# Performance work log

Measured on AMD Instinct MI355X. Metric: run time of the kernel, lower is better.

The kernel has to match this reference:

```python
import jax, jax.numpy as jnp
import numpy as np

N_SRC, N_DST, E = 10000, 10000, 640000
S, T, O, H = 128, 128, 128, 4
D = O // H


def setup_inputs() -> dict:
    key = jax.random.key(0)
    ks = jax.random.split(key, 12)
    f = lambda k, shape, fan: jax.random.normal(k, shape, dtype=jnp.float32) / np.float32(np.sqrt(fan))
    return {
        "x_src": jax.random.normal(ks[0], (N_SRC, S), dtype=jnp.float32),
        "x_dst": jax.random.normal(ks[1], (N_DST, T), dtype=jnp.float32),
        "W_pred1": f(ks[2], (S, T), T),
        "b_pred1": jnp.zeros((S,), jnp.float32),
        "W_pred2": f(ks[3], (S, S), S),
        "b_pred2": jnp.zeros((S,), jnp.float32),
        "W_res": f(ks[4], (H * D, S), S),
        "W_src": f(ks[5], (H * D, S), S),
        "W_dst": f(ks[6], (H * D, T), T),
        "att_src": jax.random.normal(ks[7], (1, H, D), dtype=jnp.float32) * 0.01,
        "att_dst": jax.random.normal(ks[8], (1, H, D), dtype=jnp.float32) * 0.01,
        "W_self": f(ks[9], (H * D, T), T),
        "b_self": jnp.zeros((H * D,), jnp.float32),
        "edge_src": jax.random.randint(ks[10], (E,), 0, N_SRC),
        "edge_dst": jax.random.randint(ks[11], (E,), 0, N_DST),
        "num_dst": N_DST,
    }


def reference(x_src, x_dst, W_pred1, b_pred1, W_pred2, b_pred2, W_res, W_src, W_dst,
              att_src, att_dst, W_self, b_self, edge_src, edge_dst, num_dst):
    h, d = att_src.shape[1], att_src.shape[2]
    # residual prediction path: pred_mlp(x_dst) = Lin2(ReLU(Lin1(x_dst)))
    pred = jax.nn.relu(x_dst @ W_pred1.T + b_pred1) @ W_pred2.T + b_pred2  # [Ndst,S]
    residual = x_src[edge_src] - pred[edge_dst]                            # [E,S]
    # per-node attention logits (equivalent to gather-then-dot, cheaper)
    a_s = ((x_src @ W_src.T).reshape(-1, h, d) * att_src).sum(-1)          # [Nsrc,H]
    a_d = ((x_dst @ W_dst.T).reshape(-1, h, d) * att_dst).sum(-1)          # [Ndst,H]
    alpha = jax.nn.leaky_relu(a_s[edge_src] + a_d[edge_dst], 0.2)          # [E,H]
    # edge softmax over incoming edges of each destination node
    amax = jax.ops.segment_max(alpha, edge_dst, num_segments=num_dst)      # [Ndst,H]
    ex = jnp.exp(alpha - amax[edge_dst])
    denom = jax.ops.segment_sum(ex, edge_dst, num_segments=num_dst)
    alpha = ex / (denom[edge_dst] + 1e-16)                                 # [E,H]
    # attention-weighted aggregation of transformed residuals
    msg = (residual @ W_res.T).reshape(-1, h, d) * alpha[:, :, None]       # [E,H,D]
    agg = jax.ops.segment_sum(msg.reshape(-1, h * d), edge_dst, num_segments=num_dst)
    return agg + x_dst @ W_self.T + b_self                                 # [Ndst,H*D]
```

## Files before the change

kernel.cpp:

```cpp
#include <hip/hip_runtime.h>

#define LEAKY 0.2f
#define CAP 160
#define CAPB 8192
#define CHUNK 2048
#define GSTRIDE 32

#define FMA4(A, S, V) do { (A).x += (S)*(V).x; (A).y += (S)*(V).y; (A).z += (S)*(V).z; (A).w += (S)*(V).w; } while (0)

struct GemmJob { const float* X; const float* W; const float* B; float* Y; int M; int relu; int bf16out; };

__device__ __forceinline__ unsigned short f2bf(float f) {
  unsigned int u = __float_as_uint(f);
  u += 0x7FFFu + ((u >> 16) & 1u);
  return (unsigned short)(u >> 16);
}
__device__ __forceinline__ float bf2f(unsigned short h) {
  return __uint_as_float(((unsigned int)h) << 16);
}

__device__ __forceinline__ void gemm128_block(
    const float* __restrict__ X, const float* __restrict__ W,
    const float* __restrict__ B, float* __restrict__ Y,
    int M, int relu, int bf16out, int row0,
    float* __restrict__ XsT , float* __restrict__ WTs ) {
  if (row0 >= M) return;
  const int tid = threadIdx.x;
  const int tx = tid & 15;
  const int ty = tid >> 4;
  float4 acc[8][2];
#pragma unroll
  for (int i = 0; i < 8; i++) {
    acc[i][0] = make_float4(0.f, 0.f, 0.f, 0.f);
    acc[i][1] = make_float4(0.f, 0.f, 0.f, 0.f);
  }
  const int rS = tid >> 1;
  const int kb = (tid & 1) * 8;

  for (int k0 = 0; k0 < 128; k0 += 16) {
    int rr = row0 + rS; if (rr >= M) rr = M - 1;
    const float* xp = X + (size_t)rr * 128 + k0 + kb;
    float4 a0 = *(const float4*)xp;
    float4 a1 = *(const float4*)(xp + 4);
    XsT[(kb + 0) * 128 + rS] = a0.x; XsT[(kb + 1) * 128 + rS] = a0.y;
    XsT[(kb + 2) * 128 + rS] = a0.z; XsT[(kb + 3) * 128 + rS] = a0.w;
    XsT[(kb + 4) * 128 + rS] = a1.x; XsT[(kb + 5) * 128 + rS] = a1.y;
    XsT[(kb + 6) * 128 + rS] = a1.z; XsT[(kb + 7) * 128 + rS] = a1.w;

    const float* wp = W + (size_t)rS * 128 + k0 + kb;
    float4 b0 = *(const float4*)wp;
    float4 b1 = *(const float4*)(wp + 4);
    WTs[(kb + 0) * 128 + rS] = b0.x; WTs[(kb + 1) * 128 + rS] = b0.y;
    WTs[(kb + 2) * 128 + rS] = b0.z; WTs[(kb + 3) * 128 + rS] = b0.w;
    WTs[(kb + 4) * 128 + rS] = b1.x; WTs[(kb + 5) * 128 + rS] = b1.y;
    WTs[(kb + 6) * 128 + rS] = b1.z; WTs[(kb + 7) * 128 + rS] = b1.w;
    __syncthreads();

#pragma unroll
    for (int k = 0; k < 16; k++) {
      float4 xa = *(const float4*)&XsT[k * 128 + ty * 4];
      float4 xb = *(const float4*)&XsT[k * 128 + 64 + ty * 4];
      float4 w0 = *(const float4*)&WTs[k * 128 + tx * 4];
      float4 w1 = *(const float4*)&WTs[k * 128 + 64 + tx * 4];
      FMA4(acc[0][0], xa.x, w0); FMA4(acc[0][1], xa.x, w1);
      FMA4(acc[1][0], xa.y, w0); FMA4(acc[1][1], xa.y, w1);
      FMA4(acc[2][0], xa.z, w0); FMA4(acc[2][1], xa.z, w1);
      FMA4(acc[3][0], xa.w, w0); FMA4(acc[3][1], xa.w, w1);
      FMA4(acc[4][0], xb.x, w0); FMA4(acc[4][1], xb.x, w1);
      FMA4(acc[5][0], xb.y, w0); FMA4(acc[5][1], xb.y, w1);
      FMA4(acc[6][0], xb.z, w0); FMA4(acc[6][1], xb.z, w1);
      FMA4(acc[7][0], xb.w, w0); FMA4(acc[7][1], xb.w, w1);
    }
    __syncthreads();
  }

  float4 bv0 = make_float4(0.f, 0.f, 0.f, 0.f);
  float4 bv1 = make_float4(0.f, 0.f, 0.f, 0.f);
  if (B) { bv0 = *(const float4*)(B + tx * 4); bv1 = *(const float4*)(B + 64 + tx * 4); }
#pragma unroll
  for (int i = 0; i < 8; i++) {
    int r = row0 + (i < 4 ? ty * 4 + i : 64 + ty * 4 + (i - 4));
    if (r < M) {
      float4 o0, o1;
      o0.x = acc[i][0].x + bv0.x; o0.y = acc[i][0].y + bv0.y;
      o0.z = acc[i][0].z + bv0.z; o0.w = acc[i][0].w + bv0.w;
      o1.x = acc[i][1].x + bv1.x; o1.y = acc[i][1].y + bv1.y;
      o1.z = acc[i][1].z + bv1.z; o1.w = acc[i][1].w + bv1.w;
      if (relu) {
        o0.x = fmaxf(o0.x, 0.f); o0.y = fmaxf(o0.y, 0.f);
        o0.z = fmaxf(o0.z, 0.f); o0.w = fmaxf(o0.w, 0.f);
        o1.x = fmaxf(o1.x, 0.f); o1.y = fmaxf(o1.y, 0.f);
        o1.z = fmaxf(o1.z, 0.f); o1.w = fmaxf(o1.w, 0.f);
      }
      if (bf16out) {
        unsigned short* yb = (unsigned short*)Y;
        ushort4 p0, p1;
        p0.x = f2bf(o0.x); p0.y = f2bf(o0.y); p0.z = f2bf(o0.z); p0.w = f2bf(o0.w);
        p1.x = f2bf(o1.x); p1.y = f2bf(o1.y); p1.z = f2bf(o1.z); p1.w = f2bf(o1.w);
        *(ushort4*)(yb + (size_t)r * 128 + tx * 4) = p0;
        *(ushort4*)(yb + (size_t)r * 128 + 64 + tx * 4) = p1;
      } else {
        *(float4*)(Y + (size_t)r * 128 + tx * 4) = o0;
        *(float4*)(Y + (size_t)r * 128 + 64 + tx * 4) = o1;
      }
    }
  }
}

__device__ __forceinline__ void attn32_block(const float* __restrict__ X,
                                             const float* __restrict__ v,
                                             float* __restrict__ a, int M, int blk,
                                             float* __restrict__ vsf ) {
  int tid = threadIdx.x;
  for (int i = tid; i < 512; i += 256) vsf[i + ((i >> 5) << 2)] = v[i];
  __syncthreads();
  int g = tid >> 3, l = tid & 7;
  int n = blk * 32 + g;
  if (n >= M) return;
  const float* xp = X + (size_t)n * 128 + l * 16;
  float4 x0 = *(const float4*)xp;
  float4 x1 = *(const float4*)(xp + 4);
  float4 x2 = *(const float4*)(xp + 8);
  float4 x3 = *(const float4*)(xp + 12);
  const float4* vv = (const float4*)vsf;
  int s = l * 18;
  float4 p = make_float4(0.f, 0.f, 0.f, 0.f);
  FMA4(p, x0.x, vv[s + 0]); FMA4(p, x0.y, vv[s + 1]); FMA4(p, x0.z, vv[s + 2]); FMA4(p, x0.w, vv[s + 3]);
  FMA4(p, x1.x, vv[s + 4]); FMA4(p, x1.y, vv[s + 5]); FMA4(p, x1.z, vv[s + 6]); FMA4(p, x1.w, vv[s + 7]);
  FMA4(p, x2.x, vv[s + 9]); FMA4(p, x2.y, vv[s +10]); FMA4(p, x2.z, vv[s +11]); FMA4(p, x2.w, vv[s +12]);
  FMA4(p, x3.x, vv[s +13]); FMA4(p, x3.y, vv[s +14]); FMA4(p, x3.z, vv[s +15]); FMA4(p, x3.w, vv[s +16]);
#pragma unroll
  for (int off = 1; off < 8; off <<= 1) {
    p.x += __shfl_xor(p.x, off, 64);
    p.y += __shfl_xor(p.y, off, 64);
    p.z += __shfl_xor(p.z, off, 64);
    p.w += __shfl_xor(p.w, off, 64);
  }
  if (l == 0) *(float4*)(a + (size_t)n * 4) = p;
}

__global__ __launch_bounds__(256) void phase1(
    const float* __restrict__ Wsrc, const float* __restrict__ attsrc,
    const float* __restrict__ Wdst, const float* __restrict__ attdst,
    const float* __restrict__ W_res, const float* __restrict__ W2,
    const float* __restrict__ b2,
    GemmJob jA,
    float* __restrict__ v_src, float* __restrict__ v_dst,
    float* __restrict__ Wc, float* __restrict__ bc,
    const int* __restrict__ edge_src, const int* __restrict__ edge_dst,
    int* __restrict__ gcnt, int* __restrict__ bin,
    int E, int Nd, int NB, int GA, int Q1, int T1) {
  __shared__ float smem[4096];
  int bx = blockIdx.x, tid = threadIdx.x;
  int u = (bx & 7) * Q1 + (bx >> 3);
  if (u >= T1) return;
  if (u == 0) {
    int which = tid >> 7, k = tid & 127;
    const float* W = which ? Wdst : Wsrc;
    const float* att = which ? attdst : attsrc;
    float* v = which ? v_dst : v_src;
    float s[4] = {0.f, 0.f, 0.f, 0.f};
#pragma unroll
    for (int h = 0; h < 4; h++)
      for (int d = 0; d < 32; d++)
        s[h] += W[(size_t)(h * 32 + d) * 128 + k] * att[h * 32 + d];
#pragma unroll
    for (int h = 0; h < 4; h++) v[k * 4 + h] = s[h];
  } else if (u == 1) {
    if (tid < 128) {
      float s = 0.f;
      for (int i = 0; i < 128; i++) s += W_res[(size_t)tid * 128 + i] * b2[i];
      bc[tid] = s;
    }
  } else if (u < 66) {
    int id = (u - 2) * 256 + tid;
    int o = id >> 7, j = id & 127;
    float s = 0.f;
    for (int i = 0; i < 128; i++) s += W_res[(size_t)o * 128 + i] * W2[(size_t)i * 128 + j];
    Wc[(size_t)o * 128 + j] = s;
  } else if (u < 66 + GA) {
    gemm128_block(jA.X, jA.W, jA.B, jA.Y, jA.M, jA.relu, jA.bf16out,
                  (u - 66) * 128, smem, smem + 2048);
  } else {
    int* pk    = (int*)smem;
    int* hist  = (int*)smem + CHUNK;
    int* gbase = hist + 160;
    int* lcur  = gbase + 160;
    int e0 = (u - 66 - GA) * CHUNK;
    int n = E - e0; if (n > CHUNK) n = CHUNK;
    if (n <= 0) return;
    for (int i = tid; i < NB; i += 256) hist[i] = 0;
    __syncthreads();
    for (int i = tid; i < n; i += 256) {
      int s = edge_src[e0 + i], d = edge_dst[e0 + i];
      pk[i] = (s << 14) | d;
      atomicAdd(&hist[d >> 6], 1);
    }
    __syncthreads();
    for (int b = tid; b < NB; b += 256) {
      gbase[b] = hist[b] ? atomicAdd(&gcnt[b * GSTRIDE], hist[b]) : 0;
      lcur[b] = 0;
    }
    __syncthreads();
    for (int i = tid; i < n; i += 256) {
      int p = pk[i];
      int b = (p & 16383) >> 6;
      int off = gbase[b] + atomicAdd(&lcur[b], 1);
      if (off < CAPB) bin[(size_t)b * CAPB + off] = p;
    }
  }
}

__global__ __launch_bounds__(256) void phase2(
    GemmJob j0, GemmJob j1, GemmJob j2,
    const float* __restrict__ x_src, const float* __restrict__ x_dst,
    const float* __restrict__ v_src, const float* __restrict__ v_dst,
    float* __restrict__ a_s, float* __restrict__ a_d,
    const int* __restrict__ gcnt, const int* __restrict__ bin,
    int* __restrict__ sorted_src, int* __restrict__ rstart, int* __restrict__ rend,
    int Ns, int Nd, int NB, int G, int As, int Ad, int Q2, int T2) {
  __shared__ float smem[4096];
  int bx = blockIdx.x, tid = threadIdx.x;
  int u = (bx % 6) * Q2 + bx / 6;
  if (u >= T2) return;
  if (u < 3 * G) {
    GemmJob J = (u < G) ? j0 : (u < 2 * G) ? j1 : j2;
    gemm128_block(J.X, J.W, J.B, J.Y, J.M, J.relu, J.bf16out, (u % G) * 128, smem, smem + 2048);
  } else if (u < 3 * G + As) {
    attn32_block(x_src, v_src, a_s, Ns, u - 3 * G, smem);
  } else if (u < 3 * G + As + Ad) {
    attn32_block(x_dst, v_dst, a_d, Nd, u - 3 * G - As, smem);
  } else {
    int b = u - (3 * G + As + Ad);
    int* hist2 = (int*)smem;
    int* lcur2 = (int*)smem + 64;
    int cnt = gcnt[b * GSTRIDE]; if (cnt > CAPB) cnt = CAPB;
    size_t base = (size_t)b * CAPB;
    if (tid < 64) hist2[tid] = 0;
    __syncthreads();
    for (int i = tid; i < cnt; i += 256) atomicAdd(&hist2[bin[base + i] & 63], 1);
    __syncthreads();
    if (tid < 64) {
      int v = hist2[tid];
      int incl = v;
#pragma unroll
      for (int off = 1; off < 64; off <<= 1) {
        int t = __shfl_up(incl, off, 64);
        if (tid >= off) incl += t;
      }
      int st = incl - v;
      lcur2[tid] = st;
      int dst = (b << 6) + tid;
      if (dst < Nd) {
        rstart[dst] = (int)base + st;
        rend[dst]   = (int)base + st + v;
      }
    }
    __syncthreads();
    for (int i = tid; i < cnt; i += 256) {
      int p = bin[base + i];
      int j = p & 63;
      int lp = atomicAdd(&lcur2[j], 1);
      sorted_src[base + lp] = p >> 14;
    }
  }
}

__global__ __launch_bounds__(256) void phase3(
    const int* __restrict__ rstart, const int* __restrict__ rend,
    const int* __restrict__ sorted_src,
    const float* __restrict__ a_s, const float* __restrict__ a_d,
    const unsigned short* __restrict__ u_src, const float* __restrict__ u_pred,
    const float* __restrict__ self_o, float* __restrict__ out, int Nd) {
  __shared__ float smem[1920];
  int bx = blockIdx.x, tid = threadIdx.x;
  int half = tid >> 7;
  int t = tid & 127;
  int dst = bx * 2 + half;
  if (dst >= Nd) return;

  float* wbuf  = smem + half * 640;
  int* srcbuf  = (int*)(smem + 1280) + half * 160;
  float4* red4 = (float4*)(smem + 1600);
  float4* redv = (float4*)(smem + 1616) + half * 32;
  float* inv_s = smem + 1872 + half * 4;
  float* sA_s  = smem + 1880 + half * 4;

  int start = rstart[dst];
  int deg = rend[dst] - start;
  float4 ad4 = *(const float4*)(a_d + (size_t)dst * 4);
  float s0 = 0.f, s1 = 0.f, s2 = 0.f, s3 = 0.f;
  for (int i = t; i < deg; i += 128) {
    int src = sorted_src[start + i];
    float4 as4 = *(const float4*)(a_s + (size_t)src * 4);
    float l0 = as4.x + ad4.x; l0 = l0 > 0.f ? l0 : LEAKY * l0;
    float l1 = as4.y + ad4.y; l1 = l1 > 0.f ? l1 : LEAKY * l1;
    float l2 = as4.z + ad4.z; l2 = l2 > 0.f ? l2 : LEAKY * l2;
    float l3 = as4.w + ad4.w; l3 = l3 > 0.f ? l3 : LEAKY * l3;
    float w0 = __expf(l0), w1 = __expf(l1), w2 = __expf(l2), w3 = __expf(l3);
    if (i < CAP) {
      wbuf[i * 4 + 0] = w0; wbuf[i * 4 + 1] = w1;
      wbuf[i * 4 + 2] = w2; wbuf[i * 4 + 3] = w3;
      srcbuf[i] = src;
    }
    s0 += w0; s1 += w1; s2 += w2; s3 += w3;
  }
  int wave = tid >> 6;
#pragma unroll
  for (int off = 32; off > 0; off >>= 1) {
    s0 += __shfl_xor(s0, off, 64);
    s1 += __shfl_xor(s1, off, 64);
    s2 += __shfl_xor(s2, off, 64);
    s3 += __shfl_xor(s3, off, 64);
  }
  if ((tid & 63) == 0) red4[wave] = make_float4(s0, s1, s2, s3);
  __syncthreads();
  if (t == 0) {
    float4 A = red4[half * 2], B = red4[half * 2 + 1];
    float dx = A.x + B.x, dy = A.y + B.y, dz = A.z + B.z, dw = A.w + B.w;
    inv_s[0] = 1.f / (dx + 1e-16f); sA_s[0] = dx * inv_s[0];
    inv_s[1] = 1.f / (dy + 1e-16f); sA_s[1] = dy * inv_s[1];
    inv_s[2] = 1.f / (dz + 1e-16f); sA_s[2] = dz * inv_s[2];
    inv_s[3] = 1.f / (dw + 1e-16f); sA_s[3] = dw * inv_s[3];
  }
  __syncthreads();

  int c4 = t & 31, rgrp = t >> 5, h = c4 >> 3;
  int coff = c4 * 4;
  float4 acc0 = make_float4(0.f,0.f,0.f,0.f), acc1 = acc0, acc2 = acc0, acc3 = acc0;
  int cap = deg < CAP ? deg : CAP;
  int i = rgrp;
  for (; i + 12 < cap; i += 16) {
    int sA = srcbuf[i], sB = srcbuf[i + 4], sC = srcbuf[i + 8], sD = srcbuf[i + 12];
    float wA = wbuf[i * 4 + h], wB = wbuf[(i + 4) * 4 + h];
    float wC = wbuf[(i + 8) * 4 + h], wD = wbuf[(i + 12) * 4 + h];
    ushort4 hA = *(const ushort4*)(u_src + (size_t)sA * 128 + coff);
    ushort4 hB = *(const ushort4*)(u_src + (size_t)sB * 128 + coff);
    ushort4 hC = *(const ushort4*)(u_src + (size_t)sC * 128 + coff);
    ushort4 hD = *(const ushort4*)(u_src + (size_t)sD * 128 + coff);
    float4 uA = make_float4(bf2f(hA.x), bf2f(hA.y), bf2f(hA.z), bf2f(hA.w));
    float4 uB = make_float4(bf2f(hB.x), bf2f(hB.y), bf2f(hB.z), bf2f(hB.w));
    float4 uC = make_float4(bf2f(hC.x), bf2f(hC.y), bf2f(hC.z), bf2f(hC.w));
    float4 uD = make_float4(bf2f(hD.x), bf2f(hD.y), bf2f(hD.z), bf2f(hD.w));
    FMA4(acc0, wA, uA); FMA4(acc1, wB, uB); FMA4(acc2, wC, uC); FMA4(acc3, wD, uD);
  }
  for (; i < cap; i += 4) {
    int s_ = srcbuf[i];
    float w = wbuf[i * 4 + h];
    ushort4 hh = *(const ushort4*)(u_src + (size_t)s_ * 128 + coff);
    float4 uu = make_float4(bf2f(hh.x), bf2f(hh.y), bf2f(hh.z), bf2f(hh.w));
    FMA4(acc0, w, uu);
  }
  if (deg > CAP) {
    float adh = (h == 0) ? ad4.x : (h == 1) ? ad4.y : (h == 2) ? ad4.z : ad4.w;
    for (int k = CAP + rgrp; k < deg; k += 4) {
      int src = sorted_src[start + k];
      float l = a_s[(size_t)src * 4 + h] + adh;
      l = l > 0.f ? l : LEAKY * l;
      float w = __expf(l);
      ushort4 hh = *(const ushort4*)(u_src + (size_t)src * 128 + coff);
      float4 uu = make_float4(bf2f(hh.x), bf2f(hh.y), bf2f(hh.z), bf2f(hh.w));
      FMA4(acc0, w, uu);
    }
  }
  float4 acc;
  acc.x = acc0.x + acc1.x + acc2.x + acc3.x;
  acc.y = acc0.y + acc1.y + acc2.y + acc3.y;
  acc.z = acc0.z + acc1.z + acc2.z + acc3.z;
  acc.w = acc0.w + acc1.w + acc2.w + acc3.w;
  acc.x += __shfl_xor(acc.x, 32, 64);
  acc.y += __shfl_xor(acc.y, 32, 64);
  acc.z += __shfl_xor(acc.z, 32, 64);
  acc.w += __shfl_xor(acc.w, 32, 64);
  if (t >= 64 && t < 96) redv[c4] = acc;
  __syncthreads();
  if (t < 32) {
    float4 r = redv[c4];
    acc.x += r.x; acc.y += r.y; acc.z += r.z; acc.w += r.w;
    float4 up = *(const float4*)(u_pred + (size_t)dst * 128 + coff);
    float4 so = *(const float4*)(self_o + (size_t)dst * 128 + coff);
    float iv = inv_s[h], sa = sA_s[h];
    float4 o;
    o.x = acc.x * iv - sa * up.x + so.x;
    o.y = acc.y * iv - sa * up.y + so.y;
    o.z = acc.z * iv - sa * up.z + so.z;
    o.w = acc.w * iv - sa * up.w + so.w;
    *(float4*)(out + (size_t)dst * 128 + coff) = o;
  }
}

extern "C" void kernel_launch(void* const* d_in, const int* in_sizes, int n_in,
                              void* d_out, int out_size, void* d_ws, size_t ws_size,
                              hipStream_t stream) {
  const float* x_src   = (const float*)d_in[0];
  const float* x_dst   = (const float*)d_in[1];
  const float* W_pred1 = (const float*)d_in[2];
  const float* b_pred1 = (const float*)d_in[3];
  const float* W_pred2 = (const float*)d_in[4];
  const float* b_pred2 = (const float*)d_in[5];
  const float* W_res   = (const float*)d_in[6];
  const float* W_src   = (const float*)d_in[7];
  const float* W_dst   = (const float*)d_in[8];
  const float* att_src = (const float*)d_in[9];
  const float* att_dst = (const float*)d_in[10];
  const float* W_self  = (const float*)d_in[11];
  const float* b_self  = (const float*)d_in[12];
  const int* edge_src  = (const int*)d_in[13];
  const int* edge_dst  = (const int*)d_in[14];
  int Ns = in_sizes[0] / 128;
  int Nd = in_sizes[1] / 128;
  int E  = in_sizes[13];
  float* out = (float*)d_out;
  int NB = (Nd + 63) >> 6;

  char* ws = (char*)d_ws;
  auto alloc = [&](size_t bytes) -> char* {
    char* p = ws;
    ws += (bytes + 255) & ~(size_t)255;
    return p;
  };
  float* relu1  = (float*)alloc((size_t)Nd * 128 * 4);
  unsigned short* u_src = (unsigned short*)alloc((size_t)Ns * 128 * 2);
  float* u_pred = (float*)alloc((size_t)Nd * 128 * 4);
  float* self_o = (float*)alloc((size_t)Nd * 128 * 4);
  float* a_s    = (float*)alloc((size_t)Ns * 4 * 4);
  float* a_d    = (float*)alloc((size_t)Nd * 4 * 4);
  float* v_src  = (float*)alloc(128 * 4 * 4);
  float* v_dst  = (float*)alloc(128 * 4 * 4);
  float* Wc     = (float*)alloc(128 * 128 * 4);
  float* bc     = (float*)alloc(128 * 4);
  int* gcnt     = (int*)alloc((size_t)NB * GSTRIDE * 4);
  int* rstart   = (int*)alloc((size_t)Nd * 4);
  int* rend     = (int*)alloc((size_t)Nd * 4);
  int* bin      = (int*)alloc((size_t)NB * CAPB * 4);
  int* sorted_src = (int*)alloc((size_t)NB * CAPB * 4);

  hipMemsetAsync(gcnt, 0, (size_t)NB * GSTRIDE * sizeof(int), stream);

  int GA  = (Nd + 127) / 128;
  int NCH = (E + CHUNK - 1) / CHUNK;
  int T1 = 66 + GA + NCH;
  int Q1 = (T1 + 7) / 8;
  GemmJob jA{ x_dst, W_pred1, b_pred1, relu1, Nd, 1, 0 };
  hipLaunchKernelGGL(phase1, dim3(Q1 * 8), dim3(256), 0, stream,
                     W_src, att_src, W_dst, att_dst, W_res, W_pred2, b_pred2, jA,
                     v_src, v_dst, Wc, bc, edge_src, edge_dst, gcnt, bin,
                     E, Nd, NB, GA, Q1, T1);

  int maxM = Ns > Nd ? Ns : Nd;
  int G  = (maxM + 127) / 128;
  int As = (Ns + 31) / 32;
  int Ad = (Nd + 31) / 32;
  int T2 = 3 * G + As + Ad + NB;
  int Q2 = (T2 + 5) / 6;
  GemmJob jB{ x_src, W_res,  nullptr, (float*)u_src, Ns, 0, 1 };
  GemmJob jC{ x_dst, W_self, b_self,  self_o, Nd, 0, 0 };
  GemmJob jU{ relu1, Wc,     bc,      u_pred, Nd, 0, 0 };
  hipLaunchKernelGGL(phase2, dim3(Q2 * 6), dim3(256), 0, stream,
                     jB, jC, jU, x_src, x_dst, v_src, v_dst, a_s, a_d,
                     gcnt, bin, sorted_src, rstart, rend,
                     Ns, Nd, NB, G, As, Ad, Q2, T2);

  hipLaunchKernelGGL(phase3, dim3((Nd + 1) / 2), dim3(256), 0, stream,
                     rstart, rend, sorted_src, a_s, a_d, u_src, u_pred, self_o, out, Nd);
}
```

Measured before the change: 166.2 us.

## Switch dense GEMMs to bf16 MFMA and fuse attention logits into GEMM

Replaces the LDS-tiled fp32 FMA GEMM with a register-only bf16 MFMA (16x16x32) GEMM that loads X and W straight from global memory and converts them to bf16 in registers. The per-node attention-logit dot products (a_s, a_d) are computed inside the x_src and x_dst GEMM blocks from the same X loads, which removes the separate attn32 blocks and their second read of X. Shared-memory use in both kernels shrinks, which may allow more resident blocks. In exchange, GEMM inputs lose precision through bf16 rounding, and the output stores are now scalar and strided instead of float4.

```diff
diff --git a/kernel.cpp b/kernel.cpp
--- a/kernel.cpp
+++ b/kernel.cpp
@@ -1,4 +1,5 @@
 #include <hip/hip_runtime.h>
+#include <hip/hip_bf16.h>
 
 #define LEAKY 0.2f
 #define CAP 160
@@ -8,7 +9,15 @@
 
 #define FMA4(A, S, V) do { (A).x += (S)*(V).x; (A).y += (S)*(V).y; (A).z += (S)*(V).z; (A).w += (S)*(V).w; } while (0)
 
-struct GemmJob { const float* X; const float* W; const float* B; float* Y; int M; int relu; int bf16out; };
+typedef __attribute__((ext_vector_type(8))) short bf16x8;
+typedef __attribute__((ext_vector_type(4))) float f32x4;
+
+struct GemmJob {
+  const float* X; const float* W; const float* B; float* Y;
+  int M; int relu; int bf16out;
+  const float* vvec;
+  float* aout;
+};
 
 __device__ __forceinline__ unsigned short f2bf(float f) {
   unsigned int u = __float_as_uint(f);
@@ -19,124 +28,127 @@
   return __uint_as_float(((unsigned int)h) << 16);
 }
 
-__device__ __forceinline__ void gemm128_block(
+__device__ __forceinline__ bf16x8 pack8(const float4& a, const float4& b) {
+  bf16x8 r;
+  r[0] = (short)__builtin_bit_cast(unsigned short, __float2bfloat16(a.x));
+  r[1] = (short)__builtin_bit_cast(unsigned short, __float2bfloat16(a.y));
+  r[2] = (short)__builtin_bit_cast(unsigned short, __float2bfloat16(a.z));
+  r[3] = (short)__builtin_bit_cast(unsigned short, __float2bfloat16(a.w));
+  r[4] = (short)__builtin_bit_cast(unsigned short, __float2bfloat16(b.x));
+  r[5] = (short)__builtin_bit_cast(unsigned short, __float2bfloat16(b.y));
+  r[6] = (short)__builtin_bit_cast(unsigned short, __float2bfloat16(b.z));
+  r[7] = (short)__builtin_bit_cast(unsigned short, __float2bfloat16(b.w));
+  return r;
+}
+
+__device__ __forceinline__ void gemm128_mfma(
     const float* __restrict__ X, const float* __restrict__ W,
     const float* __restrict__ B, float* __restrict__ Y,
     int M, int relu, int bf16out, int row0,
-    float* __restrict__ XsT , float* __restrict__ WTs ) {
+    const float* __restrict__ vvec, float* __restrict__ aout) {
   if (row0 >= M) return;
   const int tid = threadIdx.x;
-  const int tx = tid & 15;
-  const int ty = tid >> 4;
-  float4 acc[8][2];
-#pragma unroll
-  for (int i = 0; i < 8; i++) {
-    acc[i][0] = make_float4(0.f, 0.f, 0.f, 0.f);
-    acc[i][1] = make_float4(0.f, 0.f, 0.f, 0.f);
-  }
-  const int rS = tid >> 1;
-  const int kb = (tid & 1) * 8;
-
-  for (int k0 = 0; k0 < 128; k0 += 16) {
-    int rr = row0 + rS; if (rr >= M) rr = M - 1;
-    const float* xp = X + (size_t)rr * 128 + k0 + kb;
-    float4 a0 = *(const float4*)xp;
-    float4 a1 = *(const float4*)(xp + 4);
-    XsT[(kb + 0) * 128 + rS] = a0.x; XsT[(kb + 1) * 128 + rS] = a0.y;
-    XsT[(kb + 2) * 128 + rS] = a0.z; XsT[(kb + 3) * 128 + rS] = a0.w;
-    XsT[(kb + 4) * 128 + rS] = a1.x; XsT[(kb + 5) * 128 + rS] = a1.y;
-    XsT[(kb + 6) * 128 + rS] = a1.z; XsT[(kb + 7) * 128 + rS] = a1.w;
-
-    const float* wp = W + (size_t)rS * 128 + k0 + kb;
-    float4 b0 = *(const float4*)wp;
-    float4 b1 = *(const float4*)(wp + 4);
-    WTs[(kb + 0) * 128 + rS] = b0.x; WTs[(kb + 1) * 128 + rS] = b0.y;
-    WTs[(kb + 2) * 128 + rS] = b0.z; WTs[(kb + 3) * 128 + rS] = b0.w;
-    WTs[(kb + 4) * 128 + rS] = b1.x; WTs[(kb + 5) * 128 + rS] = b1.y;
-    WTs[(kb + 6) * 128 + rS] = b1.z; WTs[(kb + 7) * 128 + rS] = b1.w;
-    __syncthreads();
-
-#pragma unroll
-    for (int k = 0; k < 16; k++) {
-      float4 xa = *(const float4*)&XsT[k * 128 + ty * 4];
-      float4 xb = *(const float4*)&XsT[k * 128 + 64 + ty * 4];
-      float4 w0 = *(const float4*)&WTs[k * 128 + tx * 4];
-      float4 w1 = *(const float4*)&WTs[k * 128 + 64 + tx * 4];
-      FMA4(acc[0][0], xa.x, w0); FMA4(acc[0][1], xa.x, w1);
-      FMA4(acc[1][0], xa.y, w0); FMA4(acc[1][1], xa.y, w1);
-      FMA4(acc[2][0], xa.z, w0); FMA4(acc[2][1], xa.z, w1);
-      FMA4(acc[3][0], xa.w, w0); FMA4(acc[3][1], xa.w, w1);
-      FMA4(acc[4][0], xb.x, w0); FMA4(acc[4][1], xb.x, w1);
-      FMA4(acc[5][0], xb.y, w0); FMA4(acc[5][1], xb.y, w1);
-      FMA4(acc[6][0], xb.z, w0); FMA4(acc[6][1], xb.z, w1);
-      FMA4(acc[7][0], xb.w, w0); FMA4(acc[7][1], xb.w, w1);
-    }
-    __syncthreads();
-  }
-
-  float4 bv0 = make_float4(0.f, 0.f, 0.f, 0.f);
-  float4 bv1 = make_float4(0.f, 0.f, 0.f, 0.f);
-  if (B) { bv0 = *(const float4*)(B + tx * 4); bv1 = *(const float4*)(B + 64 + tx * 4); }
-#pragma unroll
-  for (int i = 0; i < 8; i++) {
-    int r = row0 + (i < 4 ? ty * 4 + i : 64 + ty * 4 + (i - 4));
-    if (r < M) {
-      float4 o0, o1;
-      o0.x = acc[i][0].x + bv0.x; o0.y = acc[i][0].y + bv0.y;
-      o0.z = acc[i][0].z + bv0.z; o0.w = acc[i][0].w + bv0.w;
-      o1.x = acc[i][1].x + bv1.x; o1.y = acc[i][1].y + bv1.y;
-      o1.z = acc[i][1].z + bv1.z; o1.w = acc[i][1].w + bv1.w;
-      if (relu) {
-        o0.x = fmaxf(o0.x, 0.f); o0.y = fmaxf(o0.y, 0.f);
-        o0.z = fmaxf(o0.z, 0.f); o0.w = fmaxf(o0.w, 0.f);
-        o1.x = fmaxf(o1.x, 0.f); o1.y = fmaxf(o1.y, 0.f);
-        o1.z = fmaxf(o1.z, 0.f); o1.w = fmaxf(o1.w, 0.f);
+  const int wv = tid >> 6;
+  const int ln = tid & 63;
+  const int lr = ln & 15;
+  const int kg = ln >> 4;
+
+  const f32x4 zero = {0.f, 0.f, 0.f, 0.f};
+  f32x4 acc[2][8];
+#pragma unroll
+  for (int mt = 0; mt < 2; mt++)
+#pragma unroll
+    for (int nt = 0; nt < 8; nt++) acc[mt][nt] = zero;
+
+  float4 av0 = make_float4(0.f, 0.f, 0.f, 0.f), av1 = av0;
+
+  const int r0 = row0 + wv * 32 + lr;
+  const int r1 = r0 + 16;
+  const int rc0 = r0 < M ? r0 : M - 1;
+  const int rc1 = r1 < M ? r1 : M - 1;
+  const float* xp0 = X + (size_t)rc0 * 128 + kg * 8;
+  const float* xp1 = X + (size_t)rc1 * 128 + kg * 8;
+  const float* wp  = W + (size_t)lr * 128 + kg * 8;
+
+#pragma unroll
+  for (int k0 = 0; k0 < 128; k0 += 32) {
+    float4 xa0 = *(const float4*)(xp0 + k0);
+    float4 xb0 = *(const float4*)(xp0 + k0 + 4);
+    float4 xa1 = *(const float4*)(xp1 + k0);
+    float4 xb1 = *(const float4*)(xp1 + k0 + 4);
+    bf16x8 a0 = pack8(xa0, xb0);
+    bf16x8 a1 = pack8(xa1, xb1);
+#pragma unroll
+    for (int nt = 0; nt < 8; nt++) {
+      const float* wq = wp + (size_t)nt * 16 * 128 + k0;
+      bf16x8 bw = pack8(*(const float4*)wq, *(const float4*)(wq + 4));
+      acc[0][nt] = __builtin_amdgcn_mfma_f32_16x16x32_bf16(a0, bw, acc[0][nt], 0, 0, 0);
+      acc[1][nt] = __builtin_amdgcn_mfma_f32_16x16x32_bf16(a1, bw, acc[1][nt], 0, 0, 0);
+    }
+    if (vvec) {
+      const float4* vv = (const float4*)vvec + (k0 + kg * 8);
+#pragma unroll
+      for (int j = 0; j < 4; j++) {
+        float4 v4 = vv[j];
+        float s0 = (j == 0) ? xa0.x : (j == 1) ? xa0.y : (j == 2) ? xa0.z : xa0.w;
+        float s1 = (j == 0) ? xa1.x : (j == 1) ? xa1.y : (j == 2) ? xa1.z : xa1.w;
+        FMA4(av0, s0, v4); FMA4(av1, s1, v4);
       }
+#pragma unroll
+      for (int j = 0; j < 4; j++) {
+        float4 v4 = vv[4 + j];
+        float s0 = (j == 0) ? xb0.x : (j == 1) ? xb0.y : (j == 2) ? xb0.z : xb0.w;
+        float s1 = (j == 0) ? xb1.x : (j == 1) ? xb1.y : (j == 2) ? xb1.z : xb1.w;
+        FMA4(av0, s0, v4); FMA4(av1, s1, v4);
+      }
+    }
+  }
+
+  if (vvec) {
+    av0.x += __shfl_xor(av0.x, 16, 64); av0.y += __shfl_xor(av0.y, 16, 64);
+    av0.z += __shfl_xor(av0.z, 16, 64); av0.w += __shfl_xor(av0.w, 16, 64);
+    av0.x += __shfl_xor(av0.x, 32, 64); av0.y += __shfl_xor(av0.y, 32, 64);
+    av0.z += __shfl_xor(av0.z, 32, 64); av0.w += __shfl_xor(av0.w, 32, 64);
+    av1.x += __shfl_xor(av1.x, 16, 64); av1.y += __shfl_xor(av1.y, 16, 64);
+    av1.z += __shfl_xor(av1.z, 16, 64); av1.w += __shfl_xor(av1.w, 16, 64);
+    av1.x += __shfl_xor(av1.x, 32, 64); av1.y += __shfl_xor(av1.y, 32, 64);
+    av1.z += __shfl_xor(av1.z, 32, 64); av1.w += __shfl_xor(av1.w, 32, 64);
+    if (kg == 0) {
+      if (r0 < M) *(float4*)(aout + (size_t)r0 * 4) = av0;
+      if (r1 < M) *(float4*)(aout + (size_t)r1 * 4) = av1;
+    }
+  }
+
+  float bv[8];
+#pragma unroll
+  for (int nt = 0; nt < 8; nt++) bv[nt] = B ? B[nt * 16 + lr] : 0.f;
+
+  const int rbase = row0 + wv * 32 + kg * 4;
+#pragma unroll
+  for (int mt = 0; mt < 2; mt++) {
+#pragma unroll
+    for (int i = 0; i < 4; i++) {
+      int r = rbase + mt * 16 + i;
+      if (r >= M) continue;
       if (bf16out) {
-        unsigned short* yb = (unsigned short*)Y;
-        ushort4 p0, p1;
-        p0.x = f2bf(o0.x); p0.y = f2bf(o0.y); p0.z = f2bf(o0.z); p0.w = f2bf(o0.w);
-        p1.x = f2bf(o1.x); p1.y = f2bf(o1.y); p1.z = f2bf(o1.z); p1.w = f2bf(o1.w);
-        *(ushort4*)(yb + (size_t)r * 128 + tx * 4) = p0;
-        *(ushort4*)(yb + (size_t)r * 128 + 64 + tx * 4) = p1;
+        unsigned short* yb = (unsigned short*)Y + (size_t)r * 128 + lr;
+#pragma unroll
+        for (int nt = 0; nt < 8; nt++) {
+          float o = acc[mt][nt][i] + bv[nt];
+          if (relu) o = fmaxf(o, 0.f);
+          yb[nt * 16] = f2bf(o);
+        }
       } else {
-        *(float4*)(Y + (size_t)r * 128 + tx * 4) = o0;
-        *(float4*)(Y + (size_t)r * 128 + 64 + tx * 4) = o1;
+        float* yp = Y + (size_t)r * 128 + lr;
+#pragma unroll
+        for (int nt = 0; nt < 8; nt++) {
+          float o = acc[mt][nt][i] + bv[nt];
+          if (relu) o = fmaxf(o, 0.f);
+          yp[nt * 16] = o;
+        }
       }
     }
   }
-}
-
-__device__ __forceinline__ void attn32_block(const float* __restrict__ X,
-                                             const float* __restrict__ v,
-                                             float* __restrict__ a, int M, int blk,
-                                             float* __restrict__ vsf ) {
-  int tid = threadIdx.x;
-  for (int i = tid; i < 512; i += 256) vsf[i + ((i >> 5) << 2)] = v[i];
-  __syncthreads();
-  int g = tid >> 3, l = tid & 7;
-  int n = blk * 32 + g;
-  if (n >= M) return;
-  const float* xp = X + (size_t)n * 128 + l * 16;
-  float4 x0 = *(const float4*)xp;
-  float4 x1 = *(const float4*)(xp + 4);
-  float4 x2 = *(const float4*)(xp + 8);
-  float4 x3 = *(const float4*)(xp + 12);
-  const float4* vv = (const float4*)vsf;
-  int s = l * 18;
-  float4 p = make_float4(0.f, 0.f, 0.f, 0.f);
-  FMA4(p, x0.x, vv[s + 0]); FMA4(p, x0.y, vv[s + 1]); FMA4(p, x0.z, vv[s + 2]); FMA4(p, x0.w, vv[s + 3]);
-  FMA4(p, x1.x, vv[s + 4]); FMA4(p, x1.y, vv[s + 5]); FMA4(p, x1.z, vv[s + 6]); FMA4(p, x1.w, vv[s + 7]);
-  FMA4(p, x2.x, vv[s + 9]); FMA4(p, x2.y, vv[s +10]); FMA4(p, x2.z, vv[s +11]); FMA4(p, x2.w, vv[s +12]);
-  FMA4(p, x3.x, vv[s +13]); FMA4(p, x3.y, vv[s +14]); FMA4(p, x3.z, vv[s +15]); FMA4(p, x3.w, vv[s +16]);
-#pragma unroll
-  for (int off = 1; off < 8; off <<= 1) {
-    p.x += __shfl_xor(p.x, off, 64);
-    p.y += __shfl_xor(p.y, off, 64);
-    p.z += __shfl_xor(p.z, off, 64);
-    p.w += __shfl_xor(p.w, off, 64);
-  }
-  if (l == 0) *(float4*)(a + (size_t)n * 4) = p;
 }
 
 __global__ __launch_bounds__(256) void phase1(
@@ -150,7 +162,7 @@
     const int* __restrict__ edge_src, const int* __restrict__ edge_dst,
     int* __restrict__ gcnt, int* __restrict__ bin,
     int E, int Nd, int NB, int GA, int Q1, int T1) {
-  __shared__ float smem[4096];
+  __shared__ int bsm[CHUNK + 3 * CAP];
   int bx = blockIdx.x, tid = threadIdx.x;
   int u = (bx & 7) * Q1 + (bx >> 3);
   if (u >= T1) return;
@@ -179,13 +191,13 @@
     for (int i = 0; i < 128; i++) s += W_res[(size_t)o * 128 + i] * W2[(size_t)i * 128 + j];
     Wc[(size_t)o * 128 + j] = s;
   } else if (u < 66 + GA) {
-    gemm128_block(jA.X, jA.W, jA.B, jA.Y, jA.M, jA.relu, jA.bf16out,
-                  (u - 66) * 128, smem, smem + 2048);
+    gemm128_mfma(jA.X, jA.W, jA.B, jA.Y, jA.M, jA.relu, jA.bf16out,
+                 (u - 66) * 128, jA.vvec, jA.aout);
   } else {
-    int* pk    = (int*)smem;
-    int* hist  = (int*)smem + CHUNK;
-    int* gbase = hist + 160;
-    int* lcur  = gbase + 160;
+    int* pk    = bsm;
+    int* hist  = bsm + CHUNK;
+    int* gbase = hist + CAP;
+    int* lcur  = gbase + CAP;
     int e0 = (u - 66 - GA) * CHUNK;
     int n = E - e0; if (n > CHUNK) n = CHUNK;
     if (n <= 0) return;
@@ -213,27 +225,20 @@
 
 __global__ __launch_bounds__(256) void phase2(
     GemmJob j0, GemmJob j1, GemmJob j2,
-    const float* __restrict__ x_src, const float* __restrict__ x_dst,
-    const float* __restrict__ v_src, const float* __restrict__ v_dst,
-    float* __restrict__ a_s, float* __restrict__ a_d,
     const int* __restrict__ gcnt, const int* __restrict__ bin,
     int* __restrict__ sorted_src, int* __restrict__ rstart, int* __restrict__ rend,
-    int Ns, int Nd, int NB, int G, int As, int Ad, int Q2, int T2) {
-  __shared__ float smem[4096];
+    int Nd, int G, int Q2, int T2) {
+  __shared__ int ssm[128];
   int bx = blockIdx.x, tid = threadIdx.x;
   int u = (bx % 6) * Q2 + bx / 6;
   if (u >= T2) return;
   if (u < 3 * G) {
     GemmJob J = (u < G) ? j0 : (u < 2 * G) ? j1 : j2;
-    gemm128_block(J.X, J.W, J.B, J.Y, J.M, J.relu, J.bf16out, (u % G) * 128, smem, smem + 2048);
-  } else if (u < 3 * G + As) {
-    attn32_block(x_src, v_src, a_s, Ns, u - 3 * G, smem);
-  } else if (u < 3 * G + As + Ad) {
-    attn32_block(x_dst, v_dst, a_d, Nd, u - 3 * G - As, smem);
+    gemm128_mfma(J.X, J.W, J.B, J.Y, J.M, J.relu, J.bf16out, (u % G) * 128, J.vvec, J.aout);
   } else {
-    int b = u - (3 * G + As + Ad);
-    int* hist2 = (int*)smem;
-    int* lcur2 = (int*)smem + 64;
+    int b = u - 3 * G;
+    int* hist2 = ssm;
+    int* lcur2 = ssm + 64;
     int cnt = gcnt[b * GSTRIDE]; if (cnt > CAPB) cnt = CAPB;
     size_t base = (size_t)b * CAPB;
     if (tid < 64) hist2[tid] = 0;
@@ -441,7 +446,7 @@
   int NCH = (E + CHUNK - 1) / CHUNK;
   int T1 = 66 + GA + NCH;
   int Q1 = (T1 + 7) / 8;
-  GemmJob jA{ x_dst, W_pred1, b_pred1, relu1, Nd, 1, 0 };
+  GemmJob jA{ x_dst, W_pred1, b_pred1, relu1, Nd, 1, 0, nullptr, nullptr };
   hipLaunchKernelGGL(phase1, dim3(Q1 * 8), dim3(256), 0, stream,
                      W_src, att_src, W_dst, att_dst, W_res, W_pred2, b_pred2, jA,
                      v_src, v_dst, Wc, bc, edge_src, edge_dst, gcnt, bin,
@@ -449,17 +454,14 @@
 
   int maxM = Ns > Nd ? Ns : Nd;
   int G  = (maxM + 127) / 128;
-  int As = (Ns + 31) / 32;
-  int Ad = (Nd + 31) / 32;
-  int T2 = 3 * G + As + Ad + NB;
+  int T2 = 3 * G + NB;
   int Q2 = (T2 + 5) / 6;
-  GemmJob jB{ x_src, W_res,  nullptr, (float*)u_src, Ns, 0, 1 };
-  GemmJob jC{ x_dst, W_self, b_self,  self_o, Nd, 0, 0 };
-  GemmJob jU{ relu1, Wc,     bc,      u_pred, Nd, 0, 0 };
+  GemmJob jB{ x_src, W_res,  nullptr, (float*)u_src, Ns, 0, 1, v_src, a_s };
+  GemmJob jC{ x_dst, W_self, b_self,  self_o, Nd, 0, 0, v_dst, a_d };
+  GemmJob jU{ relu1, Wc,     bc,      u_pred, Nd, 0, 0, nullptr, nullptr };
   hipLaunchKernelGGL(phase2, dim3(Q2 * 6), dim3(256), 0, stream,
-                     jB, jC, jU, x_src, x_dst, v_src, v_dst, a_s, a_d,
-                     gcnt, bin, sorted_src, rstart, rend,
-                     Ns, Nd, NB, G, As, Ad, Q2, T2);
+                     jB, jC, jU, gcnt, bin, sorted_src, rstart, rend,
+                     Nd, G, Q2, T2);
 
   hipLaunchKernelGGL(phase3, dim3((Nd + 1) / 2), dim3(256), 0, stream,
                      rstart, rend, sorted_src, a_s, a_d, u_src, u_pred, self_o, out, Nd);
```

Result: faster. 157.3 us (-5.4%).
